# Kernel optimization log

Hardware: AMD Instinct MI355X
Metric: run time of the kernel (lower is better)

Reference implementation:

```python
import jax, jax.numpy as jnp
import numpy as np
import math

EMB_ATOM = 256
PAIR_IN = 64
PAIR_OUT = 64
EMB_RBF = 16
N_ATOMS = 50000
N_EDGES = 1_600_000
KMAX = 32


def setup_inputs() -> dict:
    key = jax.random.key(0)
    ks = jax.random.split(key, 8)
    h = jax.random.normal(ks[0], (N_ATOMS, EMB_ATOM), dtype=jnp.float32)
    rad_basis = jax.random.normal(ks[1], (N_ATOMS, EMB_RBF, KMAX), dtype=jnp.float32)
    edge_index = jax.random.randint(ks[2], (2, N_EDGES), 0, N_ATOMS, dtype=jnp.int64)
    target_neighbor_idx = jax.random.randint(ks[3], (N_EDGES,), 0, KMAX, dtype=jnp.int64)
    # Learned parameters (Dense layers are bias-free); stored as [in, out].
    W_down = jax.random.normal(ks[4], (EMB_ATOM, PAIR_IN), dtype=jnp.float32) / math.sqrt(EMB_ATOM)
    W_bilinear = jax.random.normal(ks[5], (EMB_RBF * PAIR_IN, PAIR_OUT), dtype=jnp.float32) / math.sqrt(EMB_RBF * PAIR_IN)
    W_up = jax.random.normal(ks[6], (PAIR_OUT, EMB_ATOM), dtype=jnp.float32) / math.sqrt(PAIR_OUT)
    scale = jnp.ones((), dtype=jnp.float32)  # ScaleFactor learned scalar
    return {"h": h, "rad_basis": rad_basis, "edge_index": edge_index,
            "target_neighbor_idx": target_neighbor_idx, "W_down": W_down,
            "W_bilinear": W_bilinear, "W_up": W_up, "scale": scale}


def reference(h, rad_basis, edge_index, target_neighbor_idx, W_down, W_bilinear, W_up, scale):
    num_atoms = h.shape[0]
    kmax = rad_basis.shape[-1]
    pair_in = W_down.shape[-1]
    # down_projection (Dense, silu activation, no bias)
    x_b = jax.nn.silu(h @ W_down)                              # [N, pair_in]
    x_ba = x_b[edge_index[0]]                                  # [E, pair_in] gather by source atom
    # scatter edge features into padded per-atom neighbor buffer
    x2 = jnp.zeros((num_atoms, kmax, pair_in), dtype=x_ba.dtype)
    x2 = x2.at[edge_index[1], target_neighbor_idx].set(x_ba)   # [N, Kmax, pair_in]
    # rbf-weighted neighbor aggregation: batched matmul
    x_ba2 = jnp.einsum('nrk,nkd->nrd', rad_basis, x2)          # [N, rbf, pair_in]
    h_out = x_ba2.reshape(num_atoms, -1) @ W_bilinear          # bilinear Dense, no activation
    h_out = h_out * scale                                      # ScaleFactor
    return jax.nn.silu(h_out @ W_up)                           # up_projection
```

## Files before the change

kernel.cpp:

```cpp
#include <hip/hip_runtime.h>

typedef __attribute__((ext_vector_type(8))) short short8;
typedef __attribute__((ext_vector_type(4))) float floatx4;
typedef unsigned short u16;
typedef unsigned long long u64;

#define KMAXN 32

__device__ __forceinline__ u16 f2b(float f) {
    unsigned u = __builtin_bit_cast(unsigned, f);
    u += 0x7FFFu + ((u >> 16) & 1u);
    return (u16)(u >> 16);
}
__device__ __forceinline__ float silu_f(float x) {
    return x / (1.f + __expf(-x));
}

__global__ __launch_bounds__(256) void k_xpose(const float* __restrict__ Wd,
                                               const float* __restrict__ Wb,
                                               const float* __restrict__ Wu,
                                               u16* __restrict__ WdT,
                                               u16* __restrict__ WbT,
                                               u16* __restrict__ WuT) {
    int idx = blockIdx.x * 256 + threadIdx.x;
    if (idx < 16384) {
        WdT[idx] = f2b(Wd[(idx & 255) * 64 + (idx >> 8)]);
    } else if (idx < 81920) {
        int i = idx - 16384;
        WbT[i] = f2b(Wb[(i & 1023) * 64 + (i >> 10)]);
    } else {
        int i = idx - 81920;
        WuT[i] = f2b(Wu[(i & 63) * 256 + (i >> 6)]);
    }
}

__global__ __launch_bounds__(256) void k_prep(const float* __restrict__ h,
                                              const u16*   __restrict__ WdT,
                                              u16*         __restrict__ xb,
                                              const int*   __restrict__ edst,
                                              const int*   __restrict__ tni,
                                              int*         __restrict__ winner,
                                              int E, int DOWN) {
    const int tid = threadIdx.x;
    if ((int)blockIdx.x >= DOWN) {
        int e = (blockIdx.x - DOWN) * 256 + tid;
        if (e < E) atomicMax(&winner[edst[e] * KMAXN + tni[e]], e);
        return;
    }
    const int wave = tid >> 6;
    const int lane = tid & 63;
    const int m = lane & 15;
    const int q = lane >> 4;
    const long atom0 = (long)blockIdx.x * 16;

    const float* arow = h + (atom0 + m) * 256 + q * 8;
    const u16* brow = WdT + (wave * 16 + m) * 256 + q * 8;
    floatx4 acc = {0.f, 0.f, 0.f, 0.f};
#pragma unroll
    for (int kk = 0; kk < 8; ++kk) {
        float4 f0 = *reinterpret_cast<const float4*>(arow + kk * 32);
        float4 f1 = *reinterpret_cast<const float4*>(arow + kk * 32 + 4);
        short8 a;
        a[0] = (short)f2b(f0.x); a[1] = (short)f2b(f0.y);
        a[2] = (short)f2b(f0.z); a[3] = (short)f2b(f0.w);
        a[4] = (short)f2b(f1.x); a[5] = (short)f2b(f1.y);
        a[6] = (short)f2b(f1.z); a[7] = (short)f2b(f1.w);
        short8 b = *reinterpret_cast<const short8*>(brow + kk * 32);
        acc = __builtin_amdgcn_mfma_f32_16x16x32_bf16(a, b, acc, 0, 0, 0);
    }
#pragma unroll
    for (int r = 0; r < 4; ++r) {
        int row = q * 4 + r;
        xb[(atom0 + row) * 64 + wave * 16 + m] = f2b(silu_f(acc[r]));
    }
}

__global__ __launch_bounds__(256) void k_resolve(int* __restrict__ winner,
                                                 const int* __restrict__ esrc,
                                                 int n4) {
    int i = blockIdx.x * 256 + threadIdx.x;
    if (i < n4) {
        int4 w = reinterpret_cast<int4*>(winner)[i];
        w.x = (w.x >= 0) ? esrc[w.x] : -1;
        w.y = (w.y >= 0) ? esrc[w.y] : -1;
        w.z = (w.z >= 0) ? esrc[w.z] : -1;
        w.w = (w.w >= 0) ? esrc[w.w] : -1;
        reinterpret_cast<int4*>(winner)[i] = w;
    }
}

#define TL_STRIDE 1032
#define X2_PAD    68

__global__ __launch_bounds__(256) void k_fused(
        const float* __restrict__ rad,
        const u16*   __restrict__ xb,
        const int*   __restrict__ winner,
        const u16*   __restrict__ WbT,
        const u16*   __restrict__ WuT,
        const float* __restrict__ scale_p,
        float* __restrict__ out) {
    __shared__ alignas(16) u16 t_lds[16][TL_STRIDE];
    __shared__ alignas(16) u16 c2_lds[16][72];
    __shared__ alignas(16) u16 x2s[4][KMAXN][X2_PAD];

    const int tid  = threadIdx.x;
    const int wave = tid >> 6;
    const int lane = tid & 63;
    const int m = lane & 15;
    const int q = lane >> 4;
    const long atom0 = (long)blockIdx.x * 16;
    const long nbase = atom0 + wave * 4;

    const int slot = lane >> 1;
    const int half = lane & 1;

    int src[4];
#pragma unroll
    for (int a = 0; a < 4; ++a) src[a] = winner[(nbase + a) * KMAXN + slot];

    short8 ra[4];
#pragma unroll
    for (int a = 0; a < 4; ++a) {
        const float* rrow = rad + (nbase + a) * 512 + m * 32 + q * 8;
        float4 r0 = *reinterpret_cast<const float4*>(rrow);
        float4 r1 = *reinterpret_cast<const float4*>(rrow + 4);
        ra[a][0] = (short)f2b(r0.x); ra[a][1] = (short)f2b(r0.y);
        ra[a][2] = (short)f2b(r0.z); ra[a][3] = (short)f2b(r0.w);
        ra[a][4] = (short)f2b(r1.x); ra[a][5] = (short)f2b(r1.y);
        ra[a][6] = (short)f2b(r1.z); ra[a][7] = (short)f2b(r1.w);
    }

    uint4 g[4][4];
#pragma unroll
    for (int a = 0; a < 4; ++a) {
        if (src[a] >= 0) {
            const uint4* p = reinterpret_cast<const uint4*>(xb + (long)src[a] * 64 + half * 32);
            g[a][0] = p[0]; g[a][1] = p[1]; g[a][2] = p[2]; g[a][3] = p[3];
        } else {
            uint4 z = {0, 0, 0, 0};
            g[a][0] = z; g[a][1] = z; g[a][2] = z; g[a][3] = z;
        }
    }

#pragma unroll
    for (int a = 0; a < 4; ++a) {
        u64* d = reinterpret_cast<u64*>(&x2s[wave][slot][half * 32]);
        const u64* s = reinterpret_cast<const u64*>(&g[a][0]);
#pragma unroll
        for (int i = 0; i < 8; ++i) d[i] = s[i];
        asm volatile("s_waitcnt lgkmcnt(0)" ::: "memory");

#pragma unroll
        for (int c = 0; c < 4; ++c) {
            short8 bx;
#pragma unroll
            for (int j = 0; j < 8; ++j) {
                bx[j] = (short)x2s[wave][q * 8 + j][c * 16 + m];
            }
            floatx4 tz = {0.f, 0.f, 0.f, 0.f};
            tz = __builtin_amdgcn_mfma_f32_16x16x32_bf16(ra[a], bx, tz, 0, 0, 0);
#pragma unroll
            for (int r = 0; r < 4; ++r) {
                t_lds[wave * 4 + a][(q * 4 + r) * 64 + c * 16 + m] = f2b(tz[r]);
            }
        }
        asm volatile("" ::: "memory");
    }
    __syncthreads();

    floatx4 c2 = {0.f, 0.f, 0.f, 0.f};
    const u16* wbrow = WbT + (wave * 16 + m) * 1024 + q * 8;
#pragma unroll 4
    for (int kk = 0; kk < 32; ++kk) {
        short8 af = *reinterpret_cast<const short8*>(&t_lds[m][kk * 32 + q * 8]);
        short8 bf = *reinterpret_cast<const short8*>(wbrow + kk * 32);
        c2 = __builtin_amdgcn_mfma_f32_16x16x32_bf16(af, bf, c2, 0, 0, 0);
    }
    {
        float sc = scale_p[0];
#pragma unroll
        for (int r = 0; r < 4; ++r) {
            c2_lds[q * 4 + r][wave * 16 + m] = f2b(c2[r] * sc);
        }
    }
    __syncthreads();

#pragma unroll
    for (int tt = 0; tt < 4; ++tt) {
        floatx4 acc = {0.f, 0.f, 0.f, 0.f};
        const u16* wurow = WuT + (wave * 64 + tt * 16 + m) * 64 + q * 8;
#pragma unroll
        for (int ks = 0; ks < 2; ++ks) {
            short8 af = *reinterpret_cast<const short8*>(&c2_lds[m][ks * 32 + q * 8]);
            short8 bf = *reinterpret_cast<const short8*>(wurow + ks * 32);
            acc = __builtin_amdgcn_mfma_f32_16x16x32_bf16(af, bf, acc, 0, 0, 0);
        }
#pragma unroll
        for (int r = 0; r < 4; ++r) {
            out[(atom0 + q * 4 + r) * 256 + wave * 64 + tt * 16 + m] = silu_f(acc[r]);
        }
    }
}

extern "C" void kernel_launch(void* const* d_in, const int* in_sizes, int n_in,
                              void* d_out, int out_size, void* d_ws, size_t ws_size,
                              hipStream_t stream) {
    const float* h     = (const float*)d_in[0];
    const float* rad   = (const float*)d_in[1];
    const int*   eidx  = (const int*)d_in[2];
    const int*   tni   = (const int*)d_in[3];
    const float* Wd    = (const float*)d_in[4];
    const float* Wb    = (const float*)d_in[5];
    const float* Wu    = (const float*)d_in[6];
    const float* scale = (const float*)d_in[7];
    float* out         = (float*)d_out;

    const int E = in_sizes[3];
    const int N = in_sizes[0] / 256;

    u16* xb = (u16*)d_ws;
    size_t off = (size_t)N * 64 * sizeof(u16);
    int* winner = (int*)((char*)d_ws + off);
    off += (size_t)N * KMAXN * sizeof(int);
    u16* WdT = (u16*)((char*)d_ws + off);  off += 16384 * 2;
    u16* WbT = (u16*)((char*)d_ws + off);  off += 65536 * 2;
    u16* WuT = (u16*)((char*)d_ws + off);

    const int DOWN = N / 16;
    const int WIN  = (E + 255) / 256;
    const int S4   = (N * KMAXN) / 4;

    hipMemsetAsync(winner, 0xFF, (size_t)N * KMAXN * sizeof(int), stream);
    k_xpose<<<384, 256, 0, stream>>>(Wd, Wb, Wu, WdT, WbT, WuT);
    k_prep<<<DOWN + WIN, 256, 0, stream>>>(h, WdT, xb, eidx + E, tni, winner, E, DOWN);
    k_resolve<<<(S4 + 255) / 256, 256, 0, stream>>>(winner, eidx, S4);
    k_fused<<<DOWN, 256, 0, stream>>>(rad, xb, winner, WbT, WuT, scale, out);
}
```

Measured before the change: 364.3 us.

## Pack edge id and source into 64-bit atomic, drop resolve pass and memset

```diff
diff --git a/kernel.cpp b/kernel.cpp
--- a/kernel.cpp
+++ b/kernel.cpp
@@ -3,6 +3,7 @@
 typedef __attribute__((ext_vector_type(8))) short short8;
 typedef __attribute__((ext_vector_type(4))) float floatx4;
 typedef unsigned short u16;
+typedef unsigned int u32;
 typedef unsigned long long u64;
 
 #define KMAXN 32
@@ -16,35 +17,49 @@
     return x / (1.f + __expf(-x));
 }
 
-__global__ __launch_bounds__(256) void k_xpose(const float* __restrict__ Wd,
-                                               const float* __restrict__ Wb,
-                                               const float* __restrict__ Wu,
-                                               u16* __restrict__ WdT,
-                                               u16* __restrict__ WbT,
-                                               u16* __restrict__ WuT) {
-    int idx = blockIdx.x * 256 + threadIdx.x;
+__global__ __launch_bounds__(256) void k_init(const float* __restrict__ Wd,
+                                              const float* __restrict__ Wb,
+                                              const float* __restrict__ Wu,
+                                              u16* __restrict__ WdT,
+                                              u16* __restrict__ WbT2,
+                                              u16* __restrict__ WuT,
+                                              u64* __restrict__ win64,
+                                              int nslots) {
+    long idx = (long)blockIdx.x * 256 + threadIdx.x;
     if (idx < 16384) {
         WdT[idx] = f2b(Wd[(idx & 255) * 64 + (idx >> 8)]);
     } else if (idx < 81920) {
-        int i = idx - 16384;
-        WbT[i] = f2b(Wb[(i & 1023) * 64 + (i >> 10)]);
+        int i = (int)idx - 16384;
+        int n = i >> 10, s = i & 1023;
+        int d = s >> 4, rbf = s & 15;
+        WbT2[i] = f2b(Wb[(rbf * 64 + d) * 64 + n]);
+    } else if (idx < 98304) {
+        int i = (int)idx - 81920;
+        WuT[i] = f2b(Wu[(i & 63) * 256 + (i >> 6)]);
     } else {
-        int i = idx - 81920;
-        WuT[i] = f2b(Wu[(i & 63) * 256 + (i >> 6)]);
+        long z = idx - 98304;
+        if (z < nslots / 2) {
+            uint4 zero = {0, 0, 0, 0};
+            reinterpret_cast<uint4*>(win64)[z] = zero;
+        }
     }
 }
 
 __global__ __launch_bounds__(256) void k_prep(const float* __restrict__ h,
                                               const u16*   __restrict__ WdT,
                                               u16*         __restrict__ xb,
+                                              const int*   __restrict__ esrc,
                                               const int*   __restrict__ edst,
                                               const int*   __restrict__ tni,
-                                              int*         __restrict__ winner,
+                                              u64*         __restrict__ win64,
                                               int E, int DOWN) {
     const int tid = threadIdx.x;
     if ((int)blockIdx.x >= DOWN) {
         int e = (blockIdx.x - DOWN) * 256 + tid;
-        if (e < E) atomicMax(&winner[edst[e] * KMAXN + tni[e]], e);
+        if (e < E) {
+            u64 v = ((u64)(unsigned)(e + 1) << 32) | (u32)esrc[e];
+            atomicMax(&win64[(long)edst[e] * KMAXN + tni[e]], v);
+        }
         return;
     }
     const int wave = tid >> 6;
@@ -70,37 +85,22 @@
     }
 #pragma unroll
     for (int r = 0; r < 4; ++r) {
-        int row = q * 4 + r;
-        xb[(atom0 + row) * 64 + wave * 16 + m] = f2b(silu_f(acc[r]));
-    }
-}
-
-__global__ __launch_bounds__(256) void k_resolve(int* __restrict__ winner,
-                                                 const int* __restrict__ esrc,
-                                                 int n4) {
-    int i = blockIdx.x * 256 + threadIdx.x;
-    if (i < n4) {
-        int4 w = reinterpret_cast<int4*>(winner)[i];
-        w.x = (w.x >= 0) ? esrc[w.x] : -1;
-        w.y = (w.y >= 0) ? esrc[w.y] : -1;
-        w.z = (w.z >= 0) ? esrc[w.z] : -1;
-        w.w = (w.w >= 0) ? esrc[w.w] : -1;
-        reinterpret_cast<int4*>(winner)[i] = w;
-    }
-}
-
-#define TL_STRIDE 1032
-#define X2_PAD    68
+        xb[(atom0 + q * 4 + r) * 64 + wave * 16 + m] = f2b(silu_f(acc[r]));
+    }
+}
+
+#define T_STRIDE 1032
+#define X2_PAD   68
 
 __global__ __launch_bounds__(256) void k_fused(
         const float* __restrict__ rad,
         const u16*   __restrict__ xb,
-        const int*   __restrict__ winner,
-        const u16*   __restrict__ WbT,
+        const u64*   __restrict__ win64,
+        const u16*   __restrict__ WbT2,
         const u16*   __restrict__ WuT,
         const float* __restrict__ scale_p,
         float* __restrict__ out) {
-    __shared__ alignas(16) u16 t_lds[16][TL_STRIDE];
+    __shared__ alignas(16) u16 t2[16][T_STRIDE];
     __shared__ alignas(16) u16 c2_lds[16][72];
     __shared__ alignas(16) u16 x2s[4][KMAXN][X2_PAD];
 
@@ -117,7 +117,10 @@
 
     int src[4];
 #pragma unroll
-    for (int a = 0; a < 4; ++a) src[a] = winner[(nbase + a) * KMAXN + slot];
+    for (int a = 0; a < 4; ++a) {
+        u64 w = win64[(nbase + a) * KMAXN + slot];
+        src[a] = w ? (int)(u32)w : -1;
+    }
 
     short8 ra[4];
 #pragma unroll
@@ -160,20 +163,20 @@
             }
             floatx4 tz = {0.f, 0.f, 0.f, 0.f};
             tz = __builtin_amdgcn_mfma_f32_16x16x32_bf16(ra[a], bx, tz, 0, 0, 0);
-#pragma unroll
-            for (int r = 0; r < 4; ++r) {
-                t_lds[wave * 4 + a][(q * 4 + r) * 64 + c * 16 + m] = f2b(tz[r]);
-            }
+            u32 lo = (u32)f2b(tz[0]) | ((u32)f2b(tz[1]) << 16);
+            u32 hi = (u32)f2b(tz[2]) | ((u32)f2b(tz[3]) << 16);
+            u64 val = (u64)lo | ((u64)hi << 32);
+            *reinterpret_cast<u64*>(&t2[wave * 4 + a][(c * 16 + m) * 16 + q * 4]) = val;
         }
         asm volatile("" ::: "memory");
     }
     __syncthreads();
 
     floatx4 c2 = {0.f, 0.f, 0.f, 0.f};
-    const u16* wbrow = WbT + (wave * 16 + m) * 1024 + q * 8;
+    const u16* wbrow = WbT2 + (wave * 16 + m) * 1024 + q * 8;
 #pragma unroll 4
     for (int kk = 0; kk < 32; ++kk) {
-        short8 af = *reinterpret_cast<const short8*>(&t_lds[m][kk * 32 + q * 8]);
+        short8 af = *reinterpret_cast<const short8*>(&t2[m][kk * 32 + q * 8]);
         short8 bf = *reinterpret_cast<const short8*>(wbrow + kk * 32);
         c2 = __builtin_amdgcn_mfma_f32_16x16x32_bf16(af, bf, c2, 0, 0, 0);
     }
@@ -218,22 +221,21 @@
 
     const int E = in_sizes[3];
     const int N = in_sizes[0] / 256;
+    const int nslots = N * KMAXN;
 
     u16* xb = (u16*)d_ws;
     size_t off = (size_t)N * 64 * sizeof(u16);
-    int* winner = (int*)((char*)d_ws + off);
-    off += (size_t)N * KMAXN * sizeof(int);
-    u16* WdT = (u16*)((char*)d_ws + off);  off += 16384 * 2;
-    u16* WbT = (u16*)((char*)d_ws + off);  off += 65536 * 2;
-    u16* WuT = (u16*)((char*)d_ws + off);
+    u64* win64 = (u64*)((char*)d_ws + off);
+    off += (size_t)nslots * sizeof(u64);
+    u16* WdT  = (u16*)((char*)d_ws + off);  off += 16384 * 2;
+    u16* WbT2 = (u16*)((char*)d_ws + off);  off += 65536 * 2;
+    u16* WuT  = (u16*)((char*)d_ws + off);
 
     const int DOWN = N / 16;
     const int WIN  = (E + 255) / 256;
-    const int S4   = (N * KMAXN) / 4;
-
-    hipMemsetAsync(winner, 0xFF, (size_t)N * KMAXN * sizeof(int), stream);
-    k_xpose<<<384, 256, 0, stream>>>(Wd, Wb, Wu, WdT, WbT, WuT);
-    k_prep<<<DOWN + WIN, 256, 0, stream>>>(h, WdT, xb, eidx + E, tni, winner, E, DOWN);
-    k_resolve<<<(S4 + 255) / 256, 256, 0, stream>>>(winner, eidx, S4);
-    k_fused<<<DOWN, 256, 0, stream>>>(rad, xb, winner, WbT, WuT, scale, out);
-}
+    const int INIT = 384 + (nslots / 2 + 255) / 256;
+
+    k_init<<<INIT, 256, 0, stream>>>(Wd, Wb, Wu, WdT, WbT2, WuT, win64, nslots);
+    k_prep<<<DOWN + WIN, 256, 0, stream>>>(h, WdT, xb, eidx, eidx + E, tni, win64, E, DOWN);
+    k_fused<<<DOWN, 256, 0, stream>>>(rad, xb, win64, WbT2, WuT, scale, out);
+}
```

Result: faster. 350.3 us (-3.8%).
